# Optimization experiments

Measured on AMD Instinct MI355X. Metric: run time of the kernel, lower is better.

## Reference

```python
import jax, jax.numpy as jnp
import numpy as np

H = 64; H2 = 32; B = 256; NPART = 64
NP = B * NPART          # 16384 part nodes
PER_TF = 512            # torque/force nodes per graph
NT = B * PER_TF; NF = NT
E = 262144              # edges per edge type
L = 5; T = 4            # 4 main hetero layers + 1 actor layer; 4 edge types
NEG = 0.2; EPS = 1e-5


def _seg_softmax(e, seg, n):
    # softmax over entries sharing the same segment id (along axis 0)
    m = jax.lax.stop_gradient(jax.ops.segment_max(e, seg, num_segments=n))
    ex = jnp.exp(e - m[seg])
    s = jax.ops.segment_sum(ex, seg, num_segments=n)
    return ex / s[seg]


def _gat(x_s, x_d, es, ed, Ws, Wd, a_s, a_d, b, n_dst):
    # PyG GATConv, heads=1, add_self_loops=False, bipartite (x_src, x_dst)
    hs = x_s @ Ws                      # [Ns,H]
    hd = x_d @ Wd                      # [Nd,H]
    e = jax.nn.leaky_relu((hs @ a_s)[es] + (hd @ a_d)[ed], NEG)   # [E]
    al = _seg_softmax(e, ed, n_dst)                                # attn per dst neighborhood
    return jax.ops.segment_sum(al[:, None] * hs[es], ed, num_segments=n_dst) + b


def _hetero_layer(xp, xt, xf, edges, Ws, Wd, a_s, a_d, b):
    # to_hetero(aggr='sum'): one GATConv per edge type, sum into each dst type
    (pts, ptd), (tps, tpd), (pfs, pfd), (fps, fpd) = edges
    out_t = _gat(xp, xt, pts, ptd, Ws[0], Wd[0], a_s[0], a_d[0], b[0], xt.shape[0])
    out_p = (_gat(xt, xp, tps, tpd, Ws[1], Wd[1], a_s[1], a_d[1], b[1], xp.shape[0])
             + _gat(xf, xp, fps, fpd, Ws[3], Wd[3], a_s[3], a_d[3], b[3], xp.shape[0]))
    out_f = _gat(xp, xf, pfs, pfd, Ws[2], Wd[2], a_s[2], a_d[2], b[2], xf.shape[0])
    return out_p, out_t, out_f


def _pool(x):
    # MultiAggregation([max, min, mean]); segments are uniform -> reshape
    xr = x.reshape(B, -1, x.shape[-1])
    return jnp.concatenate([xr.max(1), xr.min(1), xr.mean(1)], axis=-1)


def reference(mass, part_state, torque_x, force_x,
              e_pt_src, e_pt_dst, e_tp_src, e_tp_dst,
              e_pf_src, e_pf_dst, e_fp_src, e_fp_dst,
              batch, part_id,
              emb_parts_W, emb_state, W_src, W_dst, a_src, a_dst, b_conv,
              ln_gamma, ln_beta, out_a_W, out_a_b,
              innet_W, innet_b, full_W, full_b, outnet_W, outnet_b):
    edges = ((e_pt_src, e_pt_dst), (e_tp_src, e_tp_dst),
             (e_pf_src, e_pf_dst), (e_fp_src, e_fp_dst))
    idx = part_state[:, 0] + 2 * part_state[:, 1]
    xp = jnp.concatenate([mass @ emb_parts_W, emb_state[idx]], axis=-1)  # [NP,H]
    xt, xf = torque_x, force_x
    for l in range(4):  # main hetero GAT, ReLU between layers, none after last
        xp, xt, xf = _hetero_layer(xp, xt, xf, edges,
                                   W_src[l], W_dst[l], a_src[l], a_dst[l], b_conv[l])
        if l < 3:
            xp, xt, xf = jax.nn.relu(xp), jax.nn.relu(xt), jax.nn.relu(xf)
    # actor: 1-layer hetero GAT (no activation)
    ap, at, af = _hetero_layer(xp, xt, xf, edges,
                               W_src[4], W_dst[4], a_src[4], a_dst[4], b_conv[4])
    # node LayerNorm
    mu = ap.mean(-1, keepdims=True)
    var = ((ap - mu) ** 2).mean(-1, keepdims=True)
    ra = (ap - mu) / jnp.sqrt(var + EPS) * ln_gamma + ln_beta
    ra = ra @ out_a_W + out_a_b                         # [NP,2]
    soft = _seg_softmax(ra, batch, B)                   # softmax per graph, per channel
    actions = jnp.zeros((B, 2, NPART), dtype=ra.dtype).at[batch, :, part_id].set(soft)
    actions = actions.reshape(B, 2 * NPART)
    rep = jnp.concatenate([_pool(xp), _pool(xt), _pool(xf)], axis=1)   # [B, 9H]
    repV = jax.nn.gelu(rep @ innet_W + innet_b, approximate=False)
    repV = jax.nn.gelu(repV @ full_W + full_b, approximate=False)
    V = jnp.tanh(repV @ outnet_W + outnet_b)            # [B,1]
    return actions, V


def setup_inputs():
    key = jax.random.key(0)
    ks = iter(jax.random.split(key, 40))
    f32 = jnp.float32
    inp = {}
    inp['mass'] = jax.random.uniform(next(ks), (NP, 1), dtype=f32)
    inp['part_state'] = jax.random.randint(next(ks), (NP, 2), 0, 2, dtype=jnp.int32)
    inp['torque_x'] = jax.random.normal(next(ks), (NT, H), dtype=f32)
    inp['force_x'] = jax.random.normal(next(ks), (NF, H), dtype=f32)
    for name, n in [('e_pt_src', NP), ('e_pt_dst', NT), ('e_tp_src', NT), ('e_tp_dst', NP),
                    ('e_pf_src', NP), ('e_pf_dst', NF), ('e_fp_src', NF), ('e_fp_dst', NP)]:
        inp[name] = jax.random.randint(next(ks), (E,), 0, n, dtype=jnp.int32)
    inp['batch'] = (jnp.arange(NP) // NPART).astype(jnp.int32)
    inp['part_id'] = (jnp.arange(NP) % NPART).astype(jnp.int32)
    s = 1.0 / np.sqrt(H)
    inp['emb_parts_W'] = jax.random.normal(next(ks), (1, H2), dtype=f32)
    inp['emb_state'] = jax.random.normal(next(ks), (4, H2), dtype=f32)
    inp['W_src'] = jax.random.normal(next(ks), (L, T, H, H), dtype=f32) * s
    inp['W_dst'] = jax.random.normal(next(ks), (L, T, H, H), dtype=f32) * s
    inp['a_src'] = jax.random.normal(next(ks), (L, T, H), dtype=f32) * s
    inp['a_dst'] = jax.random.normal(next(ks), (L, T, H), dtype=f32) * s
    inp['b_conv'] = jax.random.normal(next(ks), (L, T, H), dtype=f32) * 0.01
    inp['ln_gamma'] = jnp.ones((H,), dtype=f32)
    inp['ln_beta'] = jnp.zeros((H,), dtype=f32)
    inp['out_a_W'] = jax.random.normal(next(ks), (H, 2), dtype=f32) * s
    inp['out_a_b'] = jnp.zeros((2,), dtype=f32)
    inp['innet_W'] = jax.random.normal(next(ks), (9 * H, H), dtype=f32) / np.sqrt(9.0 * H)
    inp['innet_b'] = jnp.zeros((H,), dtype=f32)
    inp['full_W'] = jax.random.normal(next(ks), (H, H), dtype=f32) * s
    inp['full_b'] = jnp.zeros((H,), dtype=f32)
    inp['outnet_W'] = jax.random.normal(next(ks), (H, 1), dtype=f32) * s
    inp['outnet_b'] = jnp.zeros((1,), dtype=f32)
    return inp
```

## Files before the change

### kernel.cpp

```cpp
#include <hip/hip_runtime.h>
#include <math.h>

#define NP_ 16384
#define NT_ 131072
#define NF_ 131072
#define E_  262144
#define B_  256
#define NDTOT 294912
#define E4_  1048576

#define D0 0
#define D1 131072
#define D2 147456
#define D3 278528
#define S0 0
#define S1 16384
#define S2 147456
#define S3 163840

__device__ __forceinline__ float dot4(float4 a, float4 b) {
  return a.x * b.x + a.y * b.y + a.z * b.z + a.w * b.w;
}

__device__ __forceinline__ void gather2(
// ... 67 lines not shown
      acc0.z += wa0 * xa0.z + wa1 * xa1.z + wa2 * xa2.z + wa3 * xa3.z;
      acc0.w += wa0 * xa0.w + wa1 * xa1.w + wa2 * xa2.w + wa3 * xa3.w;
      acc1.x += wb0 * xb0.x + wb1 * xb1.x + wb2 * xb2.x + wb3 * xb3.x;
      acc1.y += wb0 * xb0.y + wb1 * xb1.y + wb2 * xb2.y + wb3 * xb3.y;
      acc1.z += wb0 * xb0.z + wb1 * xb1.z + wb2 * xb2.z + wb3 * xb3.z;
      acc1.w += wb0 * xb0.w + wb1 * xb1.w + wb2 * xb2.w + wb3 * xb3.w;
    }
    m0 = mn0; m1 = mn1;
  }
  *si0o = (sum0 > 0.f) ? 1.f / sum0 : 0.f;
  *si1o = (sum1 > 0.f) ? 1.f / sum1 : 0.f;
  *acc0o = acc0;
  *acc1o = acc1;
}

__global__ void k_wa(const float* __restrict__ Wsrc, const float* __restrict__ Wdst,
                     const float* __restrict__ asrc, const float* __restrict__ adst,
                     float* __restrict__ wsas, float* __restrict__ wdad) {
  int b = blockIdx.x;
  int lt = b >> 1;
  int role = b & 1;
  int k = threadIdx.x;
  const float* W = (role == 0 ? Wsrc : Wdst) + ((size_t)(lt * 64 + k)) * 64;
  const float* a = (role == 0 ? asrc : adst) + lt * 64;
  float s = 0.f;
  for (int i = 0; i < 64; i++) s += W[i] * a[i];
  (role == 0 ? wsas : wdad)[lt * 64 + k] = s;
}

__global__ __launch_bounds__(256) void k_build_xp(const float* __restrict__ mass,
    const int* __restrict__ ps, const float* __restrict__ embW,
    const float* __restrict__ embS, const float* __restrict__ wsas,
    const float* __restrict__ wdad, float* __restrict__ xp,
    float* __restrict__ aS, float* __restrict__ aD) {
  int tid = threadIdx.x;
  int n = blockIdx.x * 16 + (tid >> 4);
  int q = tid & 15;
  float4 v;
  if (q < 8) {
    float mv = mass[n];
    const float* e = embW + q * 4;
    v.x = mv * e[0]; v.y = mv * e[1]; v.z = mv * e[2]; v.w = mv * e[3];
  } else {
    int idx = ps[n * 2] + 2 * ps[n * 2 + 1];
    const float4* e = (const float4*)(embS + idx * 32 + (q - 8) * 4);
    v = *e;
  }
  *(float4*)(xp + (size_t)n * 64 + q * 4) = v;
  float4 w0 = *(const float4*)(wsas + 0 * 64 + q * 4);
  float4 w2 = *(const float4*)(wsas + 2 * 64 + q * 4);
  float4 d1 = *(const float4*)(wdad + 1 * 64 + q * 4);
  float4 d3 = *(const float4*)(wdad + 3 * 64 + q * 4);
  float p0 = dot4(v, w0), p2 = dot4(v, w2), p1 = dot4(v, d1), p3 = dot4(v, d3);
#pragma unroll
  for (int off = 1; off < 16; off <<= 1) {
    p0 += __shfl_xor(p0, off); p2 += __shfl_xor(p2, off);
    p1 += __shfl_xor(p1, off); p3 += __shfl_xor(p3, off);
  }
  if (q == 0) { aS[S0 + n] = p0; aS[S2 + n] = p2; aD[D1 + n] = p1; aD[D3 + n] = p3; }
}

__global__ __launch_bounds__(256) void k_init_dots(const float* __restrict__ tx,
    const float* __restrict__ fx, const float* __restrict__ wsas,
    const float* __restrict__ wdad, float* __restrict__ aS, float* __restrict__ aD) {
  int tid = threadIdx.x;
  int q = tid & 15, slot = tid >> 4;
  int b = blockIdx.x;
  int isF = (b >= 8192);
  int n = (isF ? b - 8192 : b) * 16 + slot;
  const float* src = (isF ? fx : tx) + (size_t)n * 64 + q * 4;
  float4 v = *(const float4*)src;
  int tsrc = isF ? 3 : 1, tdst = isF ? 2 : 0;
  float4 ws = *(const float4*)(wsas + tsrc * 64 + q * 4);
  float4 wd = *(const float4*)(wdad + tdst * 64 + q * 4);
// ... 125 lines not shown
  int run = psum[tid] - s;
  for (int j = 0; j < per; j++) {
    int v = cnt[b0 + j];
    cnt[b0 + j] = run;
    rowptr[csr0 + b0 + j] = eb + run;
    run += v;
  }
  __syncthreads();
  for (int i = eb + tid; i < ee; i += 256) {
    int2 p = pairs[i];
    int pos = eb + atomicAdd(&cnt[p.x - rowLo], 1);
    sortsrc[pos] = p.y;
  }
}

__global__ __launch_bounds__(256) void k_part_hs(int l, const float* __restrict__ Wsrc,
    const float* __restrict__ bconv, const float* __restrict__ xt,
    const float* __restrict__ xf, const float* __restrict__ xp,
    const int* __restrict__ rowptr, const int* __restrict__ sortsrc,
    const float* __restrict__ aSrd, const float* __restrict__ aDrd,
    float* __restrict__ aSwr, float* __restrict__ aDwr,
    const float* __restrict__ wsas, const float* __restrict__ wdad,
    float* __restrict__ xpo, float* __restrict__ hs0, float* __restrict__ hs2,
    int relu, int writeDots,
    const float* __restrict__ gamma, const float* __restrict__ beta,
    const float* __restrict__ oaW, const float* __restrict__ oab,
    float* __restrict__ raOut) {
  __shared__ float Wl[4096];
  __shared__ float shC[2176];
  int tid = threadIdx.x;

  if (blockIdx.x >= NP_ / 16) {
    int b = blockIdx.x - NP_ / 16;
    const float4* W0g = (const float4*)(Wsrc + (size_t)(l * 4 + 0) * 4096);
    const float4* W2g = (const float4*)(Wsrc + (size_t)(l * 4 + 2) * 4096);
#pragma unroll
    for (int i = 0; i < 4; i++) ((float4*)Wl)[i * 256 + tid] = W0g[i * 256 + tid];
    int rlocal = tid >> 4, q = tid & 15;
    int n = b * 16 + rlocal;
    float4 xv = *(const float4*)(xp + (size_t)n * 64 + q * 4);
    *(float4*)(shC + rlocal * 68 + q * 4) = xv;
    __syncthreads();
    const float* xr = shC + rlocal * 68;
    const float4* Wc = (const float4*)Wl;
    float4 o0 = make_float4(0.f, 0.f, 0.f, 0.f);
#pragma unroll 4
    for (int k4 = 0; k4 < 16; k4++) {
      float4 a4 = *(const float4*)(xr + k4 * 4);
#pragma unroll
      for (int kk = 0; kk < 4; kk++) {
        float av = kk == 0 ? a4.x : kk == 1 ? a4.y : kk == 2 ? a4.z : a4.w;
        float4 w0 = Wc[(k4 * 4 + kk) * 16 + q];
        o0.x += av * w0.x; o0.y += av * w0.y; o0.z += av * w0.z; o0.w += av * w0.w;
      }
    }
    *(float4*)(hs0 + (size_t)n * 64 + q * 4) = o0;
    __syncthreads();
#pragma unroll
    for (int i = 0; i < 4; i++) ((float4*)Wl)[i * 256 + tid] = W2g[i * 256 + tid];
    __syncthreads();
    float4 o2 = make_float4(0.f, 0.f, 0.f, 0.f);
#pragma unroll 4
    for (int k4 = 0; k4 < 16; k4++) {
      float4 a4 = *(const float4*)(xr + k4 * 4);
#pragma unroll
      for (int kk = 0; kk < 4; kk++) {
        float av = kk == 0 ? a4.x : kk == 1 ? a4.y : kk == 2 ? a4.z : a4.w;
        float4 w2 = Wc[(k4 * 4 + kk) * 16 + q];
        o2.x += av * w2.x; o2.y += av * w2.y; o2.z += av * w2.z; o2.w += av * w2.w;
      }
    }
    *(float4*)(hs2 + (size_t)n * 64 + q * 4) = o2;
    return;
  }

  float* rowA = shC; float* rowB = shC + 1088;
  const float4* W1g = (const float4*)(Wsrc + (size_t)(l * 4 + 1) * 4096);
  const float4* W3g = (const float4*)(Wsrc + (size_t)(l * 4 + 3) * 4096);
#pragma unroll
  for (int i = 0; i < 4; i++) ((float4*)Wl)[i * 256 + tid] = W1g[i * 256 + tid];

  int rlocal = tid >> 4;
  int q = tid & 15;
  int lanebase = (tid & 63) & 48;
  int n = blockIdx.x * 16 + rlocal;
  int row1 = D1 + n;
  int row3 = D3 + n;

  {
    int kb1 = rowptr[row1], ke1 = rowptr[row1 + 1];
    int kb3 = rowptr[row3], ke3 = rowptr[row3 + 1];
    float4 accA, accB; float siA, siB;
    gather2(kb1, ke1, aDrd[row1], aSrd + S1, xt,
            kb3, ke3, aDrd[row3], aSrd + S3, xf,
            sortsrc, q, lanebase, &accA, &siA, &accB, &siB);
    accA.x *= siA; accA.y *= siA; accA.z *= siA; accA.w *= siA;
    accB.x *= siB; accB.y *= siB; accB.z *= siB; accB.w *= siB;
    *(float4*)(rowA + rlocal * 68 + q * 4) = accA;
    *(float4*)(rowB + rlocal * 68 + q * 4) = accB;
  }
  __syncthreads();

  const float* b1 = bconv + (l * 4 + 1) * 64;
  const float* b3 = bconv + (l * 4 + 3) * 64;
  float4 o = *(const float4*)(b1 + q * 4);
  float4 o3b = *(const float4*)(b3 + q * 4);
  o.x += o3b.x; o.y += o3b.y; o.z += o3b.z; o.w += o3b.w;
  const float4* Wc = (const float4*)Wl;
#pragma unroll 4
  for (int k4 = 0; k4 < 16; k4++) {
    float4 a4 = *(const float4*)(rowA + rlocal * 68 + k4 * 4);
#pragma unroll
    for (int kk = 0; kk < 4; kk++) {
      float av = kk == 0 ? a4.x : kk == 1 ? a4.y : kk == 2 ? a4.z : a4.w;
      float4 w1 = Wc[(k4 * 4 + kk) * 16 + q];
      o.x += av * w1.x; o.y += av * w1.y; o.z += av * w1.z; o.w += av * w1.w;
    }
  }
  __syncthreads();
#pragma unroll
  for (int i = 0; i < 4; i++) ((float4*)Wl)[i * 256 + tid] = W3g[i * 256 + tid];
  __syncthreads();
#pragma unroll 4
  for (int k4 = 0; k4 < 16; k4++) {
    float4 b4 = *(const float4*)(rowB + rlocal * 68 + k4 * 4);
#pragma unroll
    for (int kk = 0; kk < 4; kk++) {
      float bv = kk == 0 ? b4.x : kk == 1 ? b4.y : kk == 2 ? b4.z : b4.w;
      float4 w3 = Wc[(k4 * 4 + kk) * 16 + q];
      o.x += bv * w3.x; o.y += bv * w3.y; o.z += bv * w3.z; o.w += bv * w3.w;
    }
  }

  if (raOut) {
    float ssum = o.x + o.y + o.z + o.w;
#pragma unroll
    for (int off = 1; off < 16; off <<= 1) ssum += __shfl_xor(ssum, off);
    float mean = ssum * (1.f / 64.f);
    float dx = o.x - mean, dy = o.y - mean, dz = o.z - mean, dw = o.w - mean;
    float v2 = dx * dx + dy * dy + dz * dz + dw * dw;
#pragma unroll
    for (int off = 1; off < 16; off <<= 1) v2 += __shfl_xor(v2, off);
    float rstd = 1.f / sqrtf(v2 * (1.f / 64.f) + 1e-5f);
    float4 g4 = *(const float4*)(gamma + q * 4);
    float4 be4 = *(const float4*)(beta + q * 4);
    float y0 = dx * rstd * g4.x + be4.x;
    float y1 = dy * rstd * g4.y + be4.y;
    float y2 = dz * rstd * g4.z + be4.z;
    float y3 = dw * rstd * g4.w + be4.w;
    float4 wA = *(const float4*)(oaW + q * 8);
    float4 wB = *(const float4*)(oaW + q * 8 + 4);
    float p0 = y0 * wA.x + y1 * wA.z + y2 * wB.x + y3 * wB.z;
    float p1 = y0 * wA.y + y1 * wA.w + y2 * wB.y + y3 * wB.w;
#pragma unroll
    for (int off = 1; off < 16; off <<= 1) {
      p0 += __shfl_xor(p0, off);
      p1 += __shfl_xor(p1, off);
    }
    if (q == 0) {
      raOut[(size_t)n * 2]     = p0 + oab[0];
      raOut[(size_t)n * 2 + 1] = p1 + oab[1];
    }
    return;
  }

  if (relu) { o.x = fmaxf(o.x, 0.f); o.y = fmaxf(o.y, 0.f); o.z = fmaxf(o.z, 0.f); o.w = fmaxf(o.w, 0.f); }
  *(float4*)(xpo + (size_t)n * 64 + q * 4) = o;

  if (writeDots) {
    float4 w0 = *(const float4*)(wsas + (size_t)((l + 1) * 4 + 0) * 64 + q * 4);
    float4 w2 = *(const float4*)(wsas + (size_t)((l + 1) * 4 + 2) * 64 + q * 4);
    float4 d1 = *(const float4*)(wdad + (size_t)((l + 1) * 4 + 1) * 64 + q * 4);
    float4 d3 = *(const float4*)(wdad + (size_t)((l + 1) * 4 + 3) * 64 + q * 4);
    float p0 = dot4(o, w0), p2 = dot4(o, w2), p1 = dot4(o, d1), p3 = dot4(o, d3);
#pragma unroll
    for (int off = 1; off < 16; off <<= 1) {
      p0 += __shfl_xor(p0, off); p2 += __shfl_xor(p2, off);
      p1 += __shfl_xor(p1, off); p3 += __shfl_xor(p3, off);
    }
    if (q == 0) { aSwr[S0 + n] = p0; aSwr[S2 + n] = p2; aDwr[D1 + n] = p1; aDwr[D3 + n] = p3; }
  }
}

__global__ __launch_bounds__(256) void k_tf(int l, const float* __restrict__ hs0,
    const float* __restrict__ hs2, const float* __restrict__ bconv,
    const int* __restrict__ rowptr, const int* __restrict__ sortsrc,
    const float* __restrict__ aSrd, const float* __restrict__ aDrd,
    float* __restrict__ aSwr, float* __restrict__ aDwr,
    const float* __restrict__ wsas, const float* __restrict__ wdad,
    float* __restrict__ xt, float* __restrict__ xf, int relu) {
  int tid = threadIdx.x;
  int q = tid & 15, slot = tid >> 4;
  int lanebase = (tid & 63) & 48;
  int b = blockIdx.x;
  int isF = (b >= 4096);
  int rg0 = (isF ? b - 4096 : b) * 32 + slot;
  int rg1 = rg0 + 16;
  int csr0 = (isF ? D2 : D0) + rg0;
  int csr1 = csr0 + 16;
  const float* hs = isF ? hs2 : hs0;
  const float* aSseg = aSrd + (isF ? S2 : S0);
  int t = isF ? 2 : 0;

  int kb0 = rowptr[csr0], ke0 = rowptr[csr0 + 1];
  int kb1 = rowptr[csr1], ke1 = rowptr[csr1 + 1];
  float4 acc0, acc1; float si0, si1;
  gather2(kb0, ke0, aDrd[csr0], aSseg, hs,
          kb1, ke1, aDrd[csr1], aSseg, hs,
          sortsrc, q, lanebase, &acc0, &si0, &acc1, &si1);

  float4 bias = *(const float4*)(bconv + (size_t)(l * 4 + t) * 64 + q * 4);
  float4 o0, o1;
  o0.x = acc0.x * si0 + bias.x; o0.y = acc0.y * si0 + bias.y;
  o0.z = acc0.z * si0 + bias.z; o0.w = acc0.w * si0 + bias.w;
  o1.x = acc1.x * si1 + bias.x; o1.y = acc1.y * si1 + bias.y;
  o1.z = acc1.z * si1 + bias.z; o1.w = acc1.w * si1 + bias.w;
  if (relu) {
    o0.x = fmaxf(o0.x, 0.f); o0.y = fmaxf(o0.y, 0.f);
    o0.z = fmaxf(o0.z, 0.f); o0.w = fmaxf(o0.w, 0.f);
    o1.x = fmaxf(o1.x, 0.f); o1.y = fmaxf(o1.y, 0.f);
    o1.z = fmaxf(o1.z, 0.f); o1.w = fmaxf(o1.w, 0.f);
  }
  float* xout = isF ? xf : xt;
  *(float4*)(xout + (size_t)rg0 * 64 + q * 4) = o0;
  *(float4*)(xout + (size_t)rg1 * 64 + q * 4) = o1;

  int tsrc = isF ? 3 : 1, tdst = isF ? 2 : 0;
  float4 wsv = *(const float4*)(wsas + (size_t)((l + 1) * 4 + tsrc) * 64 + q * 4);
  float4 wdv = *(const float4*)(wdad + (size_t)((l + 1) * 4 + tdst) * 64 + q * 4);
  float pS0 = dot4(o0, wsv), pD0 = dot4(o0, wdv);
  float pS1 = dot4(o1, wsv), pD1 = dot4(o1, wdv);
#pragma unroll
  for (int off = 1; off < 16; off <<= 1) {
    pS0 += __shfl_xor(pS0, off); pD0 += __shfl_xor(pD0, off);
    pS1 += __shfl_xor(pS1, off); pD1 += __shfl_xor(pD1, off);
  }
  if (q == 0) {
    if (!isF) {
      aSwr[S1 + rg0] = pS0; aDwr[D0 + rg0] = pD0;
      aSwr[S1 + rg1] = pS1; aDwr[D0 + rg1] = pD1;
    } else {
      aSwr[S3 + rg0] = pS0; aDwr[D2 + rg0] = pD0;
      aSwr[S3 + rg1] = pS1; aDwr[D2 + rg1] = pD1;
    }
  }
}

__global__ __launch_bounds__(64) void k_actor(const float* __restrict__ ra,
                                              float* __restrict__ outp) {
  int g = blockIdx.x;
  int p = threadIdx.x;
  float2 rv = *(const float2*)(ra + (size_t)(g * 64 + p) * 2);
  float m0 = rv.x, m1 = rv.y;
  for (int off = 32; off > 0; off >>= 1) {
    m0 = fmaxf(m0, __shfl_xor(m0, off));
    m1 = fmaxf(m1, __shfl_xor(m1, off));
  }
  float e0 = __expf(rv.x - m0), e1 = __expf(rv.y - m1);
  float s0 = e0, s1 = e1;
// ... 110 lines not shown
  const float* oab   = (const float*)d_in[24];
  const float* inW   = (const float*)d_in[25];
  const float* inb   = (const float*)d_in[26];
  const float* fW    = (const float*)d_in[27];
  const float* fb    = (const float*)d_in[28];
  const float* oW    = (const float*)d_in[29];
  const float* ob    = (const float*)d_in[30];

  char* base = (char*)d_ws;
  size_t off = 0;
  auto alloc = [&](size_t bytes) -> void* {
    void* r = base + off;
    off = (off + bytes + 255) & ~(size_t)255;
    return r;
  };
  float* xp0 = (float*)alloc((size_t)NP_ * 64 * 4);
  float* xp1 = (float*)alloc((size_t)NP_ * 64 * 4);
  float* xt  = (float*)alloc((size_t)NT_ * 64 * 4);
  float* xf  = (float*)alloc((size_t)NF_ * 64 * 4);
  float* hs0 = (float*)alloc((size_t)NP_ * 64 * 4);
  float* hs2 = (float*)alloc((size_t)NP_ * 64 * 4);
  float* aSb[2], *aDb[2];
  aSb[0] = (float*)alloc((size_t)NDTOT * 4);
  aSb[1] = (float*)alloc((size_t)NDTOT * 4);
  aDb[0] = (float*)alloc((size_t)NDTOT * 4);
  aDb[1] = (float*)alloc((size_t)NDTOT * 4);
  float* wsas = (float*)alloc(1280 * 4);
  float* wdad = (float*)alloc(1280 * 4);
  float* pool = (float*)alloc((size_t)B_ * 9 * 3 * 64 * 4);
  float* ra   = (float*)alloc((size_t)NP_ * 2 * 4);
  int* rowptr = (int*)alloc((size_t)(NDTOT + 1) * 4);
  int* sortsrc = (int*)alloc((size_t)E4_ * 4);
  int2* pairs  = (int2*)alloc((size_t)E4_ * 8);
  int* counts  = (int*)alloc(16384 * 4);
  int* cbase   = (int*)alloc(16384 * 4);
  int* granBase = (int*)alloc(257 * 4);

  k_wa<<<40, 64, 0, stream>>>(Wsrc, Wdst, asrc, adst, wsas, wdad);
  k_build_xp<<<NP_ / 16, 256, 0, stream>>>(mass, ps, embW, embS, wsas, wdad,
                                           xp0, aSb[0], aDb[0]);
  k_init_dots<<<(NT_ + NF_) / 16, 256, 0, stream>>>(torque_x, force_x,
                                                    wsas, wdad, aSb[0], aDb[0]);
  k_count<<<256, 256, 0, stream>>>(ept_d, etp_d, epf_d, efp_d, counts);
  k_bases<<<1, 256, 0, stream>>>(counts, cbase, granBase, rowptr);
  k_place<<<256, 256, 0, stream>>>(ept_d, ept_s, etp_d, etp_s, epf_d, epf_s,
                                   efp_d, efp_s, cbase, pairs);
  k_build<<<256, 256, 0, stream>>>(pairs, granBase, rowptr, sortsrc);

  float* xpbuf[2] = { xp0, xp1 };
  int cur = 0;
  for (int l = 0; l < 5; l++) {
    int ri = l & 1, wi = (l + 1) & 1;
    int relu = (l < 3) ? 1 : 0;
    const float* xtr = (l == 0) ? torque_x : xt;
    const float* xfr = (l == 0) ? force_x : xf;
    int grid = (l < 4) ? (2 * NP_ / 16) : (NP_ / 16);
    k_part_hs<<<grid, 256, 0, stream>>>(l, Wsrc, bconv, xtr, xfr, xpbuf[cur],
                                        rowptr, sortsrc,
                                        aSb[ri], aDb[ri], aSb[wi], aDb[wi],
                                        wsas, wdad, xpbuf[1 - cur], hs0, hs2,
                                        relu, (l < 4) ? 1 : 0,
                                        gamma, beta, oaW, oab,
                                        (l == 4) ? ra : (float*)nullptr);
    if (l < 4)
      k_tf<<<(NT_ + NF_) / 32, 256, 0, stream>>>(l, hs0, hs2, bconv, rowptr, sortsrc,
                                                 aSb[ri], aDb[ri], aSb[wi], aDb[wi],
                                                 wsas, wdad, xt, xf, relu);
    cur = 1 - cur;
  }

  float* outp = (float*)d_out;
  k_actor<<<B_, 64, 0, stream>>>(ra, outp);
  k_pool<<<B_ * 9, 256, 0, stream>>>(xp0, xt, xf, pool);
  k_vhead<<<B_, 256, 0, stream>>>(pool, inW, inb, fW, fb, oW, ob, outp + B_ * 128);
}
```

Before: 552.5 us.

## Fuse next-layer source projections into part kernel and widen torque/force gather

The per-layer part kernel now computes the next layer's hs0/hs2 source projections directly from the freshly produced part features, held in registers. This removes the separate half of the grid that reloaded xp and recomputed projections, and double-buffers hs so the torque/force kernel reads the previous layer's projections. The initial build kernel likewise produces hs0/hs2 instead of xp. The torque/force kernel handles four destination rows per 16-lane group instead of two, halving its grid. The trade-off is more shared memory (two weight matrices), more registers, and more divergence across the four rows of different lengths.

Result: slower. 603.6 us (+9.3%).

```diff
diff --git a/kernel.cpp b/kernel.cpp
--- a/kernel.cpp
+++ b/kernel.cpp
@@ -105,6 +105,150 @@
   *acc1o = acc1;
 }
 
+__device__ __forceinline__ void gather4(
+    int kbA, int keA, float adA,
+    int kbB, int keB, float adB,
+    int kbC, int keC, float adC,
+    int kbD, int keD, float adD,
+    const float* __restrict__ aS, const float* __restrict__ x,
+    const int* __restrict__ sortsrc, int q, int lanebase,
+    float4* accAo, float* siAo, float4* accBo, float* siBo,
+    float4* accCo, float* siCo, float4* accDo, float* siDo) {
+  float4 aA = make_float4(0.f, 0.f, 0.f, 0.f);
+  float4 aB = aA, aC = aA, aDv = aA;
+  float mA = -3e38f, mB = -3e38f, mC = -3e38f, mD = -3e38f;
+  float sA = 0.f, sB = 0.f, sC = 0.f, sD = 0.f;
+  int len = max(max(keA - kbA, keB - kbB), max(keC - kbC, keD - kbD));
+  for (int c = 0; c < len; c += 16) {
+    int kA = kbA + c + q, kB = kbB + c + q, kC = kbC + c + q, kD = kbD + c + q;
+    int vA = kA < keA, vB = kB < keB, vC = kC < keC, vD = kD < keD;
+    int iA = vA ? sortsrc[kA] : 0;
+    int iB = vB ? sortsrc[kB] : 0;
+    int iC = vC ? sortsrc[kC] : 0;
+    int iD = vD ? sortsrc[kD] : 0;
+    float eA = -3e38f, eB = -3e38f, eC = -3e38f, eD = -3e38f;
+    if (vA) { float u = aS[iA] + adA; eA = u > 0.f ? u : 0.2f * u; }
+    if (vB) { float u = aS[iB] + adB; eB = u > 0.f ? u : 0.2f * u; }
+    if (vC) { float u = aS[iC] + adC; eC = u > 0.f ? u : 0.2f * u; }
+    if (vD) { float u = aS[iD] + adD; eD = u > 0.f ? u : 0.2f * u; }
+    float cA = eA, cB = eB, cC = eC, cD = eD;
+#pragma unroll
+    for (int off = 1; off < 16; off <<= 1) {
+      cA = fmaxf(cA, __shfl_xor(cA, off));
+      cB = fmaxf(cB, __shfl_xor(cB, off));
+      cC = fmaxf(cC, __shfl_xor(cC, off));
+      cD = fmaxf(cD, __shfl_xor(cD, off));
+    }
+    float nA = fmaxf(mA, cA), nB = fmaxf(mB, cB);
+    float nC = fmaxf(mC, cC), nD = fmaxf(mD, cD);
+    float wA = vA ? __expf(eA - nA) : 0.f;
+    float wB = vB ? __expf(eB - nB) : 0.f;
+    float wC = vC ? __expf(eC - nC) : 0.f;
+    float wD = vD ? __expf(eD - nD) : 0.f;
+    float uA = wA, uB = wB, uC = wC, uD = wD;
+#pragma unroll
+    for (int off = 1; off < 16; off <<= 1) {
+      uA += __shfl_xor(uA, off);
+      uB += __shfl_xor(uB, off);
+      uC += __shfl_xor(uC, off);
+      uD += __shfl_xor(uD, off);
+    }
+    float rA = __expf(mA - nA), rB = __expf(mB - nB);
+    float rC = __expf(mC - nC), rD = __expf(mD - nD);
+    sA = sA * rA + uA; sB = sB * rB + uB;
+    sC = sC * rC + uC; sD = sD * rD + uD;
+    aA.x *= rA; aA.y *= rA; aA.z *= rA; aA.w *= rA;
+    aB.x *= rB; aB.y *= rB; aB.z *= rB; aB.w *= rB;
+    aC.x *= rC; aC.y *= rC; aC.z *= rC; aC.w *= rC;
+    aDv.x *= rD; aDv.y *= rD; aDv.z *= rD; aDv.w *= rD;
+    int dA = keA - (kbA + c); dA = dA < 0 ? 0 : (dA > 16 ? 16 : dA);
+    int dB = keB - (kbB + c); dB = dB < 0 ? 0 : (dB > 16 ? 16 : dB);
+    int dC = keC - (kbC + c); dC = dC < 0 ? 0 : (dC > 16 ? 16 : dC);
+    int dD = keD - (kbD + c); dD = dD < 0 ? 0 : (dD > 16 ? 16 : dD);
+    int cmax = max(max(dA, dB), max(dC, dD));
+    for (int i = 0; i < cmax; i += 4) {
+      {
+        float w0 = __shfl(wA, lanebase + i, 64);
+        float w1 = __shfl(wA, lanebase + i + 1, 64);
+        float w2 = __shfl(wA, lanebase + i + 2, 64);
+        float w3 = __shfl(wA, lanebase + i + 3, 64);
+        int s0 = __shfl(iA, lanebase + i, 64);
+        int s1 = __shfl(iA, lanebase + i + 1, 64);
+        int s2 = __shfl(iA, lanebase + i + 2, 64);
+        int s3 = __shfl(iA, lanebase + i + 3, 64);
+        float4 x0 = *(const float4*)(x + (size_t)s0 * 64 + q * 4);
+        float4 x1 = *(const float4*)(x + (size_t)s1 * 64 + q * 4);
+        float4 x2 = *(const float4*)(x + (size_t)s2 * 64 + q * 4);
+        float4 x3 = *(const float4*)(x + (size_t)s3 * 64 + q * 4);
+        aA.x += w0 * x0.x + w1 * x1.x + w2 * x2.x + w3 * x3.x;
+        aA.y += w0 * x0.y + w1 * x1.y + w2 * x2.y + w3 * x3.y;
+        aA.z += w0 * x0.z + w1 * x1.z + w2 * x2.z + w3 * x3.z;
+        aA.w += w0 * x0.w + w1 * x1.w + w2 * x2.w + w3 * x3.w;
+      }
+      {
+        float w0 = __shfl(wB, lanebase + i, 64);
+        float w1 = __shfl(wB, lanebase + i + 1, 64);
+        float w2 = __shfl(wB, lanebase + i + 2, 64);
+        float w3 = __shfl(wB, lanebase + i + 3, 64);
+        int s0 = __shfl(iB, lanebase + i, 64);
+        int s1 = __shfl(iB, lanebase + i + 1, 64);
+        int s2 = __shfl(iB, lanebase + i + 2, 64);
+        int s3 = __shfl(iB, lanebase + i + 3, 64);
+        float4 x0 = *(const float4*)(x + (size_t)s0 * 64 + q * 4);
+        float4 x1 = *(const float4*)(x + (size_t)s1 * 64 + q * 4);
+        float4 x2 = *(const float4*)(x + (size_t)s2 * 64 + q * 4);
+        float4 x3 = *(const float4*)(x + (size_t)s3 * 64 + q * 4);
+        aB.x += w0 * x0.x + w1 * x1.x + w2 * x2.x + w3 * x3.x;
+        aB.y += w0 * x0.y + w1 * x1.y + w2 * x2.y + w3 * x3.y;
+        aB.z += w0 * x0.z + w1 * x1.z + w2 * x2.z + w3 * x3.z;
+        aB.w += w0 * x0.w + w1 * x1.w + w2 * x2.w + w3 * x3.w;
+      }
+      {
+        float w0 = __shfl(wC, lanebase + i, 64);
+        float w1 = __shfl(wC, lanebase + i + 1, 64);
+        float w2 = __shfl(wC, lanebase + i + 2, 64);
+        float w3 = __shfl(wC, lanebase + i + 3, 64);
+        int s0 = __shfl(iC, lanebase + i, 64);
+        int s1 = __shfl(iC, lanebase + i + 1, 64);
+        int s2 = __shfl(iC, lanebase + i + 2, 64);
+        int s3 = __shfl(iC, lanebase + i + 3, 64);
+        float4 x0 = *(const float4*)(x + (size_t)s0 * 64 + q * 4);
+        float4 x1 = *(const float4*)(x + (size_t)s1 * 64 + q * 4);
+        float4 x2 = *(const float4*)(x + (size_t)s2 * 64 + q * 4);
+        float4 x3 = *(const float4*)(x + (size_t)s3 * 64 + q * 4);
+        aC.x += w0 * x0.x + w1 * x1.x + w2 * x2.x + w3 * x3.x;
+        aC.y += w0 * x0.y + w1 * x1.y + w2 * x2.y + w3 * x3.y;
+        aC.z += w0 * x0.z + w1 * x1.z + w2 * x2.z + w3 * x3.z;
+        aC.w += w0 * x0.w + w1 * x1.w + w2 * x2.w + w3 * x3.w;
+      }
+      {
+        float w0 = __shfl(wD, lanebase + i, 64);
+        float w1 = __shfl(wD, lanebase + i + 1, 64);
+        float w2 = __shfl(wD, lanebase + i + 2, 64);
+        float w3 = __shfl(wD, lanebase + i + 3, 64);
+        int s0 = __shfl(iD, lanebase + i, 64);
+        int s1 = __shfl(iD, lanebase + i + 1, 64);
+        int s2 = __shfl(iD, lanebase + i + 2, 64);
+        int s3 = __shfl(iD, lanebase + i + 3, 64);
+        float4 x0 = *(const float4*)(x + (size_t)s0 * 64 + q * 4);
+        float4 x1 = *(const float4*)(x + (size_t)s1 * 64 + q * 4);
+        float4 x2 = *(const float4*)(x + (size_t)s2 * 64 + q * 4);
+        float4 x3 = *(const float4*)(x + (size_t)s3 * 64 + q * 4);
+        aDv.x += w0 * x0.x + w1 * x1.x + w2 * x2.x + w3 * x3.x;
+        aDv.y += w0 * x0.y + w1 * x1.y + w2 * x2.y + w3 * x3.y;
+        aDv.z += w0 * x0.z + w1 * x1.z + w2 * x2.z + w3 * x3.z;
+        aDv.w += w0 * x0.w + w1 * x1.w + w2 * x2.w + w3 * x3.w;
+      }
+    }
+    mA = nA; mB = nB; mC = nC; mD = nD;
+  }
+  *siAo = (sA > 0.f) ? 1.f / sA : 0.f;
+  *siBo = (sB > 0.f) ? 1.f / sB : 0.f;
+  *siCo = (sC > 0.f) ? 1.f / sC : 0.f;
+  *siDo = (sD > 0.f) ? 1.f / sD : 0.f;
+  *accAo = aA; *accBo = aB; *accCo = aC; *accDo = aDv;
+}
+
 __global__ void k_wa(const float* __restrict__ Wsrc, const float* __restrict__ Wdst,
                      const float* __restrict__ asrc, const float* __restrict__ adst,
                      float* __restrict__ wsas, float* __restrict__ wdad) {
@@ -121,12 +265,24 @@
 
 __global__ __launch_bounds__(256) void k_build_xp(const float* __restrict__ mass,
     const int* __restrict__ ps, const float* __restrict__ embW,
-    const float* __restrict__ embS, const float* __restrict__ wsas,
-    const float* __restrict__ wdad, float* __restrict__ xp,
+    const float* __restrict__ embS, const float* __restrict__ Wsrc,
+    const float* __restrict__ wsas, const float* __restrict__ wdad,
+    float* __restrict__ hs0, float* __restrict__ hs2,
     float* __restrict__ aS, float* __restrict__ aD) {
+  __shared__ float WA[4096], WB[4096];
   int tid = threadIdx.x;
   int n = blockIdx.x * 16 + (tid >> 4);
   int q = tid & 15;
+  int lanebase = (tid & 63) & 48;
+  {
+    const float4* W0g = (const float4*)(Wsrc + (size_t)0 * 4096);
+    const float4* W2g = (const float4*)(Wsrc + (size_t)2 * 4096);
+#pragma unroll
+    for (int i = 0; i < 4; i++) {
+      ((float4*)WA)[i * 256 + tid] = W0g[i * 256 + tid];
+      ((float4*)WB)[i * 256 + tid] = W2g[i * 256 + tid];
+    }
+  }
   float4 v;
   if (q < 8) {
     float mv = mass[n];
@@ -137,7 +293,6 @@
     const float4* e = (const float4*)(embS + idx * 32 + (q - 8) * 4);
     v = *e;
   }
-  *(float4*)(xp + (size_t)n * 64 + q * 4) = v;
   float4 w0 = *(const float4*)(wsas + 0 * 64 + q * 4);
   float4 w2 = *(const float4*)(wsas + 2 * 64 + q * 4);
   float4 d1 = *(const float4*)(wdad + 1 * 64 + q * 4);
@@ -149,6 +304,36 @@
     p1 += __shfl_xor(p1, off); p3 += __shfl_xor(p3, off);
   }
   if (q == 0) { aS[S0 + n] = p0; aS[S2 + n] = p2; aD[D1 + n] = p1; aD[D3 + n] = p3; }
+  __syncthreads();
+  const float4* WAc = (const float4*)WA;
+  const float4* WBc = (const float4*)WB;
+  float4 h0 = make_float4(0.f, 0.f, 0.f, 0.f);
+  float4 h2 = make_float4(0.f, 0.f, 0.f, 0.f);
+#pragma unroll 4
+  for (int k4 = 0; k4 < 16; k4++) {
+    float ax = __shfl(v.x, lanebase + k4, 64);
+    float ay = __shfl(v.y, lanebase + k4, 64);
+    float az = __shfl(v.z, lanebase + k4, 64);
+    float aw = __shfl(v.w, lanebase + k4, 64);
+    float4 a0 = WAc[(k4 * 4 + 0) * 16 + q];
+    float4 a1 = WAc[(k4 * 4 + 1) * 16 + q];
+    float4 a2 = WAc[(k4 * 4 + 2) * 16 + q];
+    float4 a3 = WAc[(k4 * 4 + 3) * 16 + q];
+    float4 c0 = WBc[(k4 * 4 + 0) * 16 + q];
+    float4 c1 = WBc[(k4 * 4 + 1) * 16 + q];
+    float4 c2 = WBc[(k4 * 4 + 2) * 16 + q];
+    float4 c3 = WBc[(k4 * 4 + 3) * 16 + q];
+    h0.x += ax * a0.x + ay * a1.x + az * a2.x + aw * a3.x;
+    h0.y += ax * a0.y + ay * a1.y + az * a2.y + aw * a3.y;
+    h0.z += ax * a0.z + ay * a1.z + az * a2.z + aw * a3.z;
+    h0.w += ax * a0.w + ay * a1.w + az * a2.w + aw * a3.w;
+    h2.x += ax * c0.x + ay * c1.x + az * c2.x + aw * c3.x;
+    h2.y += ax * c0.y + ay * c1.y + az * c2.y + aw * c3.y;
+    h2.z += ax * c0.z + ay * c1.z + az * c2.z + aw * c3.z;
+    h2.w += ax * c0.w + ay * c1.w + az * c2.w + aw * c3.w;
+  }
+  *(float4*)(hs0 + (size_t)n * 64 + q * 4) = h0;
+  *(float4*)(hs2 + (size_t)n * 64 + q * 4) = h2;
 }
 
 __global__ __launch_bounds__(256) void k_init_dots(const float* __restrict__ tx,
@@ -304,122 +489,78 @@
   }
 }
 
-__global__ __launch_bounds__(256) void k_part_hs(int l, const float* __restrict__ Wsrc,
-    const float* __restrict__ bconv, const float* __restrict__ xt,
-    const float* __restrict__ xf, const float* __restrict__ xp,
+__global__ __launch_bounds__(256) void k_part(int l,
+    const float* __restrict__ Wsrc, const float* __restrict__ bconv,
+    const float* __restrict__ xt, const float* __restrict__ xf,
     const int* __restrict__ rowptr, const int* __restrict__ sortsrc,
     const float* __restrict__ aSrd, const float* __restrict__ aDrd,
     float* __restrict__ aSwr, float* __restrict__ aDwr,
     const float* __restrict__ wsas, const float* __restrict__ wdad,
-    float* __restrict__ xpo, float* __restrict__ hs0, float* __restrict__ hs2,
-    int relu, int writeDots,
+    float* __restrict__ xpo, float* __restrict__ hs0n, float* __restrict__ hs2n,
+    int relu, int writeHs, int writeXp,
     const float* __restrict__ gamma, const float* __restrict__ beta,
     const float* __restrict__ oaW, const float* __restrict__ oab,
     float* __restrict__ raOut) {
-  __shared__ float Wl[4096];
-  __shared__ float shC[2176];
+  __shared__ float WA[4096], WB[4096];
   int tid = threadIdx.x;
-
-  if (blockIdx.x >= NP_ / 16) {
-    int b = blockIdx.x - NP_ / 16;
-    const float4* W0g = (const float4*)(Wsrc + (size_t)(l * 4 + 0) * 4096);
-    const float4* W2g = (const float4*)(Wsrc + (size_t)(l * 4 + 2) * 4096);
-#pragma unroll
-    for (int i = 0; i < 4; i++) ((float4*)Wl)[i * 256 + tid] = W0g[i * 256 + tid];
-    int rlocal = tid >> 4, q = tid & 15;
-    int n = b * 16 + rlocal;
-    float4 xv = *(const float4*)(xp + (size_t)n * 64 + q * 4);
-    *(float4*)(shC + rlocal * 68 + q * 4) = xv;
-    __syncthreads();
-    const float* xr = shC + rlocal * 68;
-    const float4* Wc = (const float4*)Wl;
-    float4 o0 = make_float4(0.f, 0.f, 0.f, 0.f);
-#pragma unroll 4
-    for (int k4 = 0; k4 < 16; k4++) {
-      float4 a4 = *(const float4*)(xr + k4 * 4);
-#pragma unroll
-      for (int kk = 0; kk < 4; kk++) {
-        float av = kk == 0 ? a4.x : kk == 1 ? a4.y : kk == 2 ? a4.z : a4.w;
-        float4 w0 = Wc[(k4 * 4 + kk) * 16 + q];
-        o0.x += av * w0.x; o0.y += av * w0.y; o0.z += av * w0.z; o0.w += av * w0.w;
-      }
-    }
-    *(float4*)(hs0 + (size_t)n * 64 + q * 4) = o0;
-    __syncthreads();
-#pragma unroll
-    for (int i = 0; i < 4; i++) ((float4*)Wl)[i * 256 + tid] = W2g[i * 256 + tid];
-    __syncthreads();
-    float4 o2 = make_float4(0.f, 0.f, 0.f, 0.f);
-#pragma unroll 4
-    for (int k4 = 0; k4 < 16; k4++) {
-      float4 a4 = *(const float4*)(xr + k4 * 4);
-#pragma unroll
-      for (int kk = 0; kk < 4; kk++) {
-        float av = kk == 0 ? a4.x : kk == 1 ? a4.y : kk == 2 ? a4.z : a4.w;
-        float4 w2 = Wc[(k4 * 4 + kk) * 16 + q];
-        o2.x += av * w2.x; o2.y += av * w2.y; o2.z += av * w2.z; o2.w += av * w2.w;
-      }
-    }
-    *(float4*)(hs2 + (size_t)n * 64 + q * 4) = o2;
-    return;
-  }
-
-  float* rowA = shC; float* rowB = shC + 1088;
-  const float4* W1g = (const float4*)(Wsrc + (size_t)(l * 4 + 1) * 4096);
-  const float4* W3g = (const float4*)(Wsrc + (size_t)(l * 4 + 3) * 4096);
-#pragma unroll
-  for (int i = 0; i < 4; i++) ((float4*)Wl)[i * 256 + tid] = W1g[i * 256 + tid];
-
-  int rlocal = tid >> 4;
   int q = tid & 15;
   int lanebase = (tid & 63) & 48;
-  int n = blockIdx.x * 16 + rlocal;
-  int row1 = D1 + n;
-  int row3 = D3 + n;
-
+  int n = blockIdx.x * 16 + (tid >> 4);
   {
-    int kb1 = rowptr[row1], ke1 = rowptr[row1 + 1];
-    int kb3 = rowptr[row3], ke3 = rowptr[row3 + 1];
-    float4 accA, accB; float siA, siB;
-    gather2(kb1, ke1, aDrd[row1], aSrd + S1, xt,
-            kb3, ke3, aDrd[row3], aSrd + S3, xf,
-            sortsrc, q, lanebase, &accA, &siA, &accB, &siB);
-    accA.x *= siA; accA.y *= siA; accA.z *= siA; accA.w *= siA;
-    accB.x *= siB; accB.y *= siB; accB.z *= siB; accB.w *= siB;
-    *(float4*)(rowA + rlocal * 68 + q * 4) = accA;
-    *(float4*)(rowB + rlocal * 68 + q * 4) = accB;
-  }
-  __syncthreads();
-
-  const float* b1 = bconv + (l * 4 + 1) * 64;
-  const float* b3 = bconv + (l * 4 + 3) * 64;
-  float4 o = *(const float4*)(b1 + q * 4);
-  float4 o3b = *(const float4*)(b3 + q * 4);
-  o.x += o3b.x; o.y += o3b.y; o.z += o3b.z; o.w += o3b.w;
-  const float4* Wc = (const float4*)Wl;
+    const float4* W1g = (const float4*)(Wsrc + (size_t)(l * 4 + 1) * 4096);
+    const float4* W3g = (const float4*)(Wsrc + (size_t)(l * 4 + 3) * 4096);
+#pragma unroll
+    for (int i = 0; i < 4; i++) {
+      ((float4*)WA)[i * 256 + tid] = W1g[i * 256 + tid];
+      ((float4*)WB)[i * 256 + tid] = W3g[i * 256 + tid];
+    }
+  }
+  __syncthreads();
+
+  int row1 = D1 + n, row3 = D3 + n;
+  int kb1 = rowptr[row1], ke1 = rowptr[row1 + 1];
+  int kb3 = rowptr[row3], ke3 = rowptr[row3 + 1];
+  float4 accA, accB; float siA, siB;
+  gather2(kb1, ke1, aDrd[row1], aSrd + S1, xt,
+          kb3, ke3, aDrd[row3], aSrd + S3, xf,
+          sortsrc, q, lanebase, &accA, &siA, &accB, &siB);
+  accA.x *= siA; accA.y *= siA; accA.z *= siA; accA.w *= siA;
+  accB.x *= siB; accB.y *= siB; accB.z *= siB; accB.w *= siB;
+
+  float4 o;
+  {
+    float4 b1 = *(const float4*)(bconv + (size_t)(l * 4 + 1) * 64 + q * 4);
+    float4 b3 = *(const float4*)(bconv + (size_t)(l * 4 + 3) * 64 + q * 4);
+    o = make_float4(b1.x + b3.x, b1.y + b3.y, b1.z + b3.z, b1.w + b3.w);
+  }
+  const float4* WAc = (const float4*)WA;
+  const float4* WBc = (const float4*)WB;
 #pragma unroll 4
   for (int k4 = 0; k4 < 16; k4++) {
-    float4 a4 = *(const float4*)(rowA + rlocal * 68 + k4 * 4);
-#pragma unroll
-    for (int kk = 0; kk < 4; kk++) {
-      float av = kk == 0 ? a4.x : kk == 1 ? a4.y : kk == 2 ? a4.z : a4.w;
-      float4 w1 = Wc[(k4 * 4 + kk) * 16 + q];
-      o.x += av * w1.x; o.y += av * w1.y; o.z += av * w1.z; o.w += av * w1.w;
-    }
-  }
-  __syncthreads();
-#pragma unroll
-  for (int i = 0; i < 4; i++) ((float4*)Wl)[i * 256 + tid] = W3g[i * 256 + tid];
-  __syncthreads();
-#pragma unroll 4
-  for (int k4 = 0; k4 < 16; k4++) {
-    float4 b4 = *(const float4*)(rowB + rlocal * 68 + k4 * 4);
-#pragma unroll
-    for (int kk = 0; kk < 4; kk++) {
-      float bv = kk == 0 ? b4.x : kk == 1 ? b4.y : kk == 2 ? b4.z : b4.w;
-      float4 w3 = Wc[(k4 * 4 + kk) * 16 + q];
-      o.x += bv * w3.x; o.y += bv * w3.y; o.z += bv * w3.z; o.w += bv * w3.w;
-    }
+    float ax = __shfl(accA.x, lanebase + k4, 64);
+    float ay = __shfl(accA.y, lanebase + k4, 64);
+    float az = __shfl(accA.z, lanebase + k4, 64);
+    float aw = __shfl(accA.w, lanebase + k4, 64);
+    float bx = __shfl(accB.x, lanebase + k4, 64);
+    float by = __shfl(accB.y, lanebase + k4, 64);
+    float bz = __shfl(accB.z, lanebase + k4, 64);
+    float bw = __shfl(accB.w, lanebase + k4, 64);
+    float4 wa0 = WAc[(k4 * 4 + 0) * 16 + q];
+    float4 wa1 = WAc[(k4 * 4 + 1) * 16 + q];
+    float4 wa2 = WAc[(k4 * 4 + 2) * 16 + q];
+    float4 wa3 = WAc[(k4 * 4 + 3) * 16 + q];
+    float4 wb0 = WBc[(k4 * 4 + 0) * 16 + q];
+    float4 wb1 = WBc[(k4 * 4 + 1) * 16 + q];
+    float4 wb2 = WBc[(k4 * 4 + 2) * 16 + q];
+    float4 wb3 = WBc[(k4 * 4 + 3) * 16 + q];
+    o.x += ax * wa0.x + ay * wa1.x + az * wa2.x + aw * wa3.x
+         + bx * wb0.x + by * wb1.x + bz * wb2.x + bw * wb3.x;
+    o.y += ax * wa0.y + ay * wa1.y + az * wa2.y + aw * wa3.y
+         + bx * wb0.y + by * wb1.y + bz * wb2.y + bw * wb3.y;
+    o.z += ax * wa0.z + ay * wa1.z + az * wa2.z + aw * wa3.z
+         + bx * wb0.z + by * wb1.z + bz * wb2.z + bw * wb3.z;
+    o.w += ax * wa0.w + ay * wa1.w + az * wa2.w + aw * wa3.w
+         + bx * wb0.w + by * wb1.w + bz * wb2.w + bw * wb3.w;
   }
 
   if (raOut) {
@@ -438,10 +579,10 @@
     float y1 = dy * rstd * g4.y + be4.y;
     float y2 = dz * rstd * g4.z + be4.z;
     float y3 = dw * rstd * g4.w + be4.w;
-    float4 wA = *(const float4*)(oaW + q * 8);
-    float4 wB = *(const float4*)(oaW + q * 8 + 4);
-    float p0 = y0 * wA.x + y1 * wA.z + y2 * wB.x + y3 * wB.z;
-    float p1 = y0 * wA.y + y1 * wA.w + y2 * wB.y + y3 * wB.w;
+    float4 wAv = *(const float4*)(oaW + q * 8);
+    float4 wBv = *(const float4*)(oaW + q * 8 + 4);
+    float p0 = y0 * wAv.x + y1 * wAv.z + y2 * wBv.x + y3 * wBv.z;
+    float p1 = y0 * wAv.y + y1 * wAv.w + y2 * wBv.y + y3 * wBv.w;
 #pragma unroll
     for (int off = 1; off < 16; off <<= 1) {
       p0 += __shfl_xor(p0, off);
@@ -455,9 +596,9 @@
   }
 
   if (relu) { o.x = fmaxf(o.x, 0.f); o.y = fmaxf(o.y, 0.f); o.z = fmaxf(o.z, 0.f); o.w = fmaxf(o.w, 0.f); }
-  *(float4*)(xpo + (size_t)n * 64 + q * 4) = o;
-
-  if (writeDots) {
+  if (writeXp) *(float4*)(xpo + (size_t)n * 64 + q * 4) = o;
+
+  {
     float4 w0 = *(const float4*)(wsas + (size_t)((l + 1) * 4 + 0) * 64 + q * 4);
     float4 w2 = *(const float4*)(wsas + (size_t)((l + 1) * 4 + 2) * 64 + q * 4);
     float4 d1 = *(const float4*)(wdad + (size_t)((l + 1) * 4 + 1) * 64 + q * 4);
@@ -469,6 +610,47 @@
       p1 += __shfl_xor(p1, off); p3 += __shfl_xor(p3, off);
     }
     if (q == 0) { aSwr[S0 + n] = p0; aSwr[S2 + n] = p2; aDwr[D1 + n] = p1; aDwr[D3 + n] = p3; }
+  }
+
+  if (writeHs) {
+    __syncthreads();
+    {
+      const float4* W0g = (const float4*)(Wsrc + (size_t)((l + 1) * 4 + 0) * 4096);
+      const float4* W2g = (const float4*)(Wsrc + (size_t)((l + 1) * 4 + 2) * 4096);
+#pragma unroll
+      for (int i = 0; i < 4; i++) {
+        ((float4*)WA)[i * 256 + tid] = W0g[i * 256 + tid];
+        ((float4*)WB)[i * 256 + tid] = W2g[i * 256 + tid];
+      }
+    }
+    __syncthreads();
+    float4 h0 = make_float4(0.f, 0.f, 0.f, 0.f);
+    float4 h2 = make_float4(0.f, 0.f, 0.f, 0.f);
+#pragma unroll 4
+    for (int k4 = 0; k4 < 16; k4++) {
+      float ox = __shfl(o.x, lanebase + k4, 64);
+      float oy = __shfl(o.y, lanebase + k4, 64);
+      float oz = __shfl(o.z, lanebase + k4, 64);
+      float ow = __shfl(o.w, lanebase + k4, 64);
+      float4 a0 = WAc[(k4 * 4 + 0) * 16 + q];
+      float4 a1 = WAc[(k4 * 4 + 1) * 16 + q];
+      float4 a2 = WAc[(k4 * 4 + 2) * 16 + q];
+      float4 a3 = WAc[(k4 * 4 + 3) * 16 + q];
+      float4 c0 = WBc[(k4 * 4 + 0) * 16 + q];
+      float4 c1 = WBc[(k4 * 4 + 1) * 16 + q];
+      float4 c2 = WBc[(k4 * 4 + 2) * 16 + q];
+      float4 c3 = WBc[(k4 * 4 + 3) * 16 + q];
+      h0.x += ox * a0.x + oy * a1.x + oz * a2.x + ow * a3.x;
+      h0.y += ox * a0.y + oy * a1.y + oz * a2.y + ow * a3.y;
+      h0.z += ox * a0.z + oy * a1.z + oz * a2.z + ow * a3.z;
+      h0.w += ox * a0.w + oy * a1.w + oz * a2.w + ow * a3.w;
+      h2.x += ox * c0.x + oy * c1.x + oz * c2.x + ow * c3.x;
+      h2.y += ox * c0.y + oy * c1.y + oz * c2.y + ow * c3.y;
+      h2.z += ox * c0.z + oy * c1.z + oz * c2.z + ow * c3.z;
+      h2.w += ox * c0.w + oy * c1.w + oz * c2.w + ow * c3.w;
+    }
+    *(float4*)(hs0n + (size_t)n * 64 + q * 4) = h0;
+    *(float4*)(hs2n + (size_t)n * 64 + q * 4) = h2;
   }
 }
 
@@ -483,56 +665,66 @@
   int q = tid & 15, slot = tid >> 4;
   int lanebase = (tid & 63) & 48;
   int b = blockIdx.x;
-  int isF = (b >= 4096);
-  int rg0 = (isF ? b - 4096 : b) * 32 + slot;
-  int rg1 = rg0 + 16;
-  int csr0 = (isF ? D2 : D0) + rg0;
-  int csr1 = csr0 + 16;
+  int isF = (b >= 2048);
+  int r0 = (isF ? b - 2048 : b) * 64 + slot;
+  int csr = (isF ? D2 : D0) + r0;
   const float* hs = isF ? hs2 : hs0;
   const float* aSseg = aSrd + (isF ? S2 : S0);
   int t = isF ? 2 : 0;
 
-  int kb0 = rowptr[csr0], ke0 = rowptr[csr0 + 1];
-  int kb1 = rowptr[csr1], ke1 = rowptr[csr1 + 1];
-  float4 acc0, acc1; float si0, si1;
-  gather2(kb0, ke0, aDrd[csr0], aSseg, hs,
-          kb1, ke1, aDrd[csr1], aSseg, hs,
-          sortsrc, q, lanebase, &acc0, &si0, &acc1, &si1);
+  int kbA = rowptr[csr],      keA = rowptr[csr + 1];
+  int kbB = rowptr[csr + 16], keB = rowptr[csr + 17];
+  int kbC = rowptr[csr + 32], keC = rowptr[csr + 33];
+  int kbD = rowptr[csr + 48], keD = rowptr[csr + 49];
+  float4 aA, aB, aC, aD4; float sA, sB, sC, sD;
+  gather4(kbA, keA, aDrd[csr],      kbB, keB, aDrd[csr + 16],
+          kbC, keC, aDrd[csr + 32], kbD, keD, aDrd[csr + 48],
+          aSseg, hs, sortsrc, q, lanebase,
+          &aA, &sA, &aB, &sB, &aC, &sC, &aD4, &sD);
 
   float4 bias = *(const float4*)(bconv + (size_t)(l * 4 + t) * 64 + q * 4);
-  float4 o0, o1;
-  o0.x = acc0.x * si0 + bias.x; o0.y = acc0.y * si0 + bias.y;
-  o0.z = acc0.z * si0 + bias.z; o0.w = acc0.w * si0 + bias.w;
-  o1.x = acc1.x * si1 + bias.x; o1.y = acc1.y * si1 + bias.y;
-  o1.z = acc1.z * si1 + bias.z; o1.w = acc1.w * si1 + bias.w;
+  float4 o0, o1, o2, o3;
+  o0.x = aA.x * sA + bias.x; o0.y = aA.y * sA + bias.y;
+  o0.z = aA.z * sA + bias.z; o0.w = aA.w * sA + bias.w;
+  o1.x = aB.x * sB + bias.x; o1.y = aB.y * sB + bias.y;
+  o1.z = aB.z * sB + bias.z; o1.w = aB.w * sB + bias.w;
+  o2.x = aC.x * sC + bias.x; o2.y = aC.y * sC + bias.y;
+  o2.z = aC.z * sC + bias.z; o2.w = aC.w * sC + bias.w;
+  o3.x = aD4.x * sD + bias.x; o3.y = aD4.y * sD + bias.y;
+  o3.z = aD4.z * sD + bias.z; o3.w = aD4.w * sD + bias.w;
   if (relu) {
-    o0.x = fmaxf(o0.x, 0.f); o0.y = fmaxf(o0.y, 0.f);
-    o0.z = fmaxf(o0.z, 0.f); o0.w = fmaxf(o0.w, 0.f);
-    o1.x = fmaxf(o1.x, 0.f); o1.y = fmaxf(o1.y, 0.f);
-    o1.z = fmaxf(o1.z, 0.f); o1.w = fmaxf(o1.w, 0.f);
+    o0.x = fmaxf(o0.x, 0.f); o0.y = fmaxf(o0.y, 0.f); o0.z = fmaxf(o0.z, 0.f); o0.w = fmaxf(o0.w, 0.f);
+    o1.x = fmaxf(o1.x, 0.f); o1.y = fmaxf(o1.y, 0.f); o1.z = fmaxf(o1.z, 0.f); o1.w = fmaxf(o1.w, 0.f);
+    o2.x = fmaxf(o2.x, 0.f); o2.y = fmaxf(o2.y, 0.f); o2.z = fmaxf(o2.z, 0.f); o2.w = fmaxf(o2.w, 0.f);
+    o3.x = fmaxf(o3.x, 0.f); o3.y = fmaxf(o3.y, 0.f); o3.z = fmaxf(o3.z, 0.f); o3.w = fmaxf(o3.w, 0.f);
   }
   float* xout = isF ? xf : xt;
-  *(float4*)(xout + (size_t)rg0 * 64 + q * 4) = o0;
-  *(float4*)(xout + (size_t)rg1 * 64 + q * 4) = o1;
+  *(float4*)(xout + (size_t)r0 * 64 + q * 4) = o0;
+  *(float4*)(xout + (size_t)(r0 + 16) * 64 + q * 4) = o1;
+  *(float4*)(xout + (size_t)(r0 + 32) * 64 + q * 4) = o2;
+  *(float4*)(xout + (size_t)(r0 + 48) * 64 + q * 4) = o3;
 
   int tsrc = isF ? 3 : 1, tdst = isF ? 2 : 0;
   float4 wsv = *(const float4*)(wsas + (size_t)((l + 1) * 4 + tsrc) * 64 + q * 4);
   float4 wdv = *(const float4*)(wdad + (size_t)((l + 1) * 4 + tdst) * 64 + q * 4);
   float pS0 = dot4(o0, wsv), pD0 = dot4(o0, wdv);
   float pS1 = dot4(o1, wsv), pD1 = dot4(o1, wdv);
+  float pS2 = dot4(o2, wsv), pD2 = dot4(o2, wdv);
+  float pS3 = dot4(o3, wsv), pD3 = dot4(o3, wdv);
 #pragma unroll
   for (int off = 1; off < 16; off <<= 1) {
     pS0 += __shfl_xor(pS0, off); pD0 += __shfl_xor(pD0, off);
     pS1 += __shfl_xor(pS1, off); pD1 += __shfl_xor(pD1, off);
+    pS2 += __shfl_xor(pS2, off); pD2 += __shfl_xor(pD2, off);
+    pS3 += __shfl_xor(pS3, off); pD3 += __shfl_xor(pD3, off);
   }
   if (q == 0) {
-    if (!isF) {
-      aSwr[S1 + rg0] = pS0; aDwr[D0 + rg0] = pD0;
-      aSwr[S1 + rg1] = pS1; aDwr[D0 + rg1] = pD1;
-    } else {
-      aSwr[S3 + rg0] = pS0; aDwr[D2 + rg0] = pD0;
-      aSwr[S3 + rg1] = pS1; aDwr[D2 + rg1] = pD1;
-    }
+    int sb = isF ? S3 : S1;
+    int db = isF ? D2 : D0;
+    aSwr[sb + r0]      = pS0; aDwr[db + r0]      = pD0;
+    aSwr[sb + r0 + 16] = pS1; aDwr[db + r0 + 16] = pD1;
+    aSwr[sb + r0 + 32] = pS2; aDwr[db + r0 + 32] = pD2;
+    aSwr[sb + r0 + 48] = pS3; aDwr[db + r0 + 48] = pD3;
   }
 }
 
@@ -673,12 +865,14 @@
     off = (off + bytes + 255) & ~(size_t)255;
     return r;
   };
-  float* xp0 = (float*)alloc((size_t)NP_ * 64 * 4);
-  float* xp1 = (float*)alloc((size_t)NP_ * 64 * 4);
+  float* xp  = (float*)alloc((size_t)NP_ * 64 * 4);
   float* xt  = (float*)alloc((size_t)NT_ * 64 * 4);
   float* xf  = (float*)alloc((size_t)NF_ * 64 * 4);
-  float* hs0 = (float*)alloc((size_t)NP_ * 64 * 4);
-  float* hs2 = (float*)alloc((size_t)NP_ * 64 * 4);
+  float* hs0b[2], *hs2b[2];
+  hs0b[0] = (float*)alloc((size_t)NP_ * 64 * 4);
+  hs0b[1] = (float*)alloc((size_t)NP_ * 64 * 4);
+  hs2b[0] = (float*)alloc((size_t)NP_ * 64 * 4);
+  hs2b[1] = (float*)alloc((size_t)NP_ * 64 * 4);
   float* aSb[2], *aDb[2];
   aSb[0] = (float*)alloc((size_t)NDTOT * 4);
   aSb[1] = (float*)alloc((size_t)NDTOT * 4);
@@ -696,8 +890,8 @@
   int* granBase = (int*)alloc(257 * 4);
 
   k_wa<<<40, 64, 0, stream>>>(Wsrc, Wdst, asrc, adst, wsas, wdad);
-  k_build_xp<<<NP_ / 16, 256, 0, stream>>>(mass, ps, embW, embS, wsas, wdad,
-                                           xp0, aSb[0], aDb[0]);
+  k_build_xp<<<NP_ / 16, 256, 0, stream>>>(mass, ps, embW, embS, Wsrc, wsas, wdad,
+                                           hs0b[0], hs2b[0], aSb[0], aDb[0]);
   k_init_dots<<<(NT_ + NF_) / 16, 256, 0, stream>>>(torque_x, force_x,
                                                     wsas, wdad, aSb[0], aDb[0]);
   k_count<<<256, 256, 0, stream>>>(ept_d, etp_d, epf_d, efp_d, counts);
@@ -706,30 +900,28 @@
                                    efp_d, efp_s, cbase, pairs);
   k_build<<<256, 256, 0, stream>>>(pairs, granBase, rowptr, sortsrc);
 
-  float* xpbuf[2] = { xp0, xp1 };
-  int cur = 0;
   for (int l = 0; l < 5; l++) {
     int ri = l & 1, wi = (l + 1) & 1;
     int relu = (l < 3) ? 1 : 0;
     const float* xtr = (l == 0) ? torque_x : xt;
     const float* xfr = (l == 0) ? force_x : xf;
-    int grid = (l < 4) ? (2 * NP_ / 16) : (NP_ / 16);
-    k_part_hs<<<grid, 256, 0, stream>>>(l, Wsrc, bconv, xtr, xfr, xpbuf[cur],
-                                        rowptr, sortsrc,
-                                        aSb[ri], aDb[ri], aSb[wi], aDb[wi],
-                                        wsas, wdad, xpbuf[1 - cur], hs0, hs2,
-                                        relu, (l < 4) ? 1 : 0,
-                                        gamma, beta, oaW, oab,
-                                        (l == 4) ? ra : (float*)nullptr);
+    k_part<<<NP_ / 16, 256, 0, stream>>>(l, Wsrc, bconv, xtr, xfr,
+                                         rowptr, sortsrc,
+                                         aSb[ri], aDb[ri], aSb[wi], aDb[wi],
+                                         wsas, wdad, xp,
+                                         hs0b[(l + 1) & 1], hs2b[(l + 1) & 1],
+                                         relu, (l < 3) ? 1 : 0, (l == 3) ? 1 : 0,
+                                         gamma, beta, oaW, oab,
+                                         (l == 4) ? ra : (float*)nullptr);
     if (l < 4)
-      k_tf<<<(NT_ + NF_) / 32, 256, 0, stream>>>(l, hs0, hs2, bconv, rowptr, sortsrc,
+      k_tf<<<(NT_ + NF_) / 64, 256, 0, stream>>>(l, hs0b[l & 1], hs2b[l & 1], bconv,
+                                                 rowptr, sortsrc,
                                                  aSb[ri], aDb[ri], aSb[wi], aDb[wi],
                                                  wsas, wdad, xt, xf, relu);
-    cur = 1 - cur;
   }
 
   float* outp = (float*)d_out;
   k_actor<<<B_, 64, 0, stream>>>(ra, outp);
-  k_pool<<<B_ * 9, 256, 0, stream>>>(xp0, xt, xf, pool);
+  k_pool<<<B_ * 9, 256, 0, stream>>>(xp, xt, xf, pool);
   k_vhead<<<B_, 256, 0, stream>>>(pool, inW, inb, fW, fb, oW, ob, outp + B_ * 128);
 }
```
